# Kernel optimization log

Hardware: AMD Instinct MI355X
Metric: run time of the kernel (lower is better)

## Reference

```python
import jax, jax.numpy as jnp
import numpy as np
from jax import lax

N_HARM = 64
N_BINS = 64
SR = 16000
B, T = 16, 64000


def setup_inputs() -> dict:
    key = jax.random.key(0)
    ks = jax.random.split(key, 12)
    audio = jax.random.normal(ks[0], (B, T), dtype=jnp.float32)
    # realistic fundamental frequencies in [80, 400) Hz
    f0 = 80.0 + 320.0 * jax.random.uniform(ks[1], (B, T), dtype=jnp.float32)
    white_noise = jax.random.normal(ks[2], (B, T), dtype=jnp.float32)
    def wconv(k, o, i, ksz):
        return jax.random.normal(k, (o, i, ksz), dtype=jnp.float32) * (1.0 / np.sqrt(i * ksz))
    w1 = wconv(ks[3], 32, 1, 9); b1 = jnp.zeros((32,), jnp.float32)
    w2 = wconv(ks[4], 64, 32, 9); b2 = jnp.zeros((64,), jnp.float32)
    w3 = wconv(ks[5], 128, 64, 9); b3 = jnp.zeros((128,), jnp.float32)
    wl = jax.random.normal(ks[6], (N_HARM + N_BINS, 128), dtype=jnp.float32) * (1.0 / np.sqrt(128))
    bl = jnp.zeros((N_HARM + N_BINS,), jnp.float32)
    return {"audio": audio, "f0": f0, "white_noise": white_noise,
            "w1": w1, "b1": b1, "w2": w2, "b2": b2, "w3": w3, "b3": b3,
            "wl": wl, "bl": bl}


def _conv1d(x, w, b):
    # x: [B, C_in, T], w: [C_out, C_in, K]; stride 2, pad 4
    y = lax.conv_general_dilated(x, w, window_strides=(2,), padding=[(4, 4)],
                                 dimension_numbers=("NCH", "OIH", "NCH"))
    return jax.nn.relu(y + b[None, :, None])


def reference(audio, f0, white_noise, w1, b1, w2, b2, w3, b3, wl, bl):
    batch, time = audio.shape
    # --- encoder ---
    x = audio[:, None, :]                    # [B, 1, T]
    x = _conv1d(x, w1, b1)                   # [B, 32, T/2]
    x = _conv1d(x, w2, b2)                   # [B, 64, T/4]
    x = _conv1d(x, w3, b3)                   # [B, 128, T/8]
    pooled = x.mean(axis=2)                  # AdaptiveAvgPool1d(1) + Flatten -> [B, 128]
    feats = pooled @ wl.T + bl               # [B, 128]
    # --- harmonic synth ---
    amps = jax.nn.relu(feats[:, :N_HARM])    # [B, H]; constant over time in original
    amps = amps / (amps.sum(axis=1, keepdims=True) + 1e-6)
    t = jnp.linspace(0.0, time / SR, time)   # endpoint-inclusive, as torch.linspace
    harm_idx = jnp.arange(1, N_HARM + 1, dtype=jnp.float32)
    # phase: [B, H, T] = 2*pi * (h * f0) * t
    phase = (2.0 * jnp.pi) * f0[:, None, :] * harm_idx[None, :, None] * t[None, None, :]
    harmonic_audio = jnp.einsum("bh,bht->bt", amps, jnp.sin(phase))
    # --- noise synth ---
    noise_mag = feats[:, N_HARM:]            # [B, n_bins]; mean over time of a constant = itself
    bin_size = time // N_BINS
    shaped = (white_noise.reshape(batch, N_BINS, bin_size) * noise_mag[:, :, None]).reshape(batch, time)
    return harmonic_audio + shaped
```

## Files before the change

### kernel.cpp

```cpp
#include <hip/hip_runtime.h>
#include <hip/hip_bf16.h>
#include <math.h>

typedef unsigned short u16;
typedef _Float16 f16x8 __attribute__((ext_vector_type(8)));
typedef float    f32x16 __attribute__((ext_vector_type(16)));
typedef u16      u16x8  __attribute__((ext_vector_type(8)));
typedef u16      u16x4  __attribute__((ext_vector_type(4)));

#define BATCH 16
#define T0 64000
#define T1 32000
#define T2 16000
#define T3 8000
#define NT3 250
#define NBLKX 32
#define NROWS1 1040

static __device__ __forceinline__ u16 f2h(float f) {
    _Float16 h = (_Float16)f;
    u16 u;
    __builtin_memcpy(&u, &h, 2);
    return u;
}

__global__ __launch_bounds__(256) void prep_w_k(const float* __restrict__ w2,
                                                const float* __restrict__ w3,
                                                u16* __restrict__ a2t,
                                                u16* __restrict__ a3t,
                                                float* __restrict__ pooled) {
    int idx = blockIdx.x * 256 + threadIdx.x;
    if (idx < 18432) {
        int j = idx & 7, o = (idx >> 3) & 63, g = (idx >> 9) & 3, kk = idx >> 11;
        a2t[idx] = f2h(w2[(o * 32 + g * 8 + j) * 9 + kk]);
    } else if (idx < 18432 + 73728) {
        int jdx = idx - 18432;
        int j = jdx & 7, o = (jdx >> 3) & 127, g = (jdx >> 10) & 7, kk = jdx >> 13;
        a3t[jdx] = f2h(w3[(o * 64 + g * 8 + j) * 9 + kk]);
    } else if (idx < 18432 + 73728 + 2048) {
        pooled[idx - 18432 - 73728] = 0.f;
    }
}

__global__ __launch_bounds__(512, 2) void mega_k(const float* __restrict__ audio,
                                                 const float* __restrict__ w1,
                                                 const float* __restrict__ b1,
                                                 const u16* __restrict__ a2t,
                                                 const float* __restrict__ b2,
                                                 const u16* __restrict__ a3t,
                                                 const float* __restrict__ b3,
                                                 float* __restrict__ pooled) {
    __shared__ u16 sm[520 * 64];
    const int tid = threadIdx.x;
    const int b = blockIdx.y;
    const int r0 = blockIdx.x * NT3;
    const int lane = tid & 63, wv = tid >> 6;
    const int ls = lane >> 5, ln = lane & 31;

    {
        const float* ar = audio + (size_t)b * T0;
        #pragma unroll
        for (int rep = 0; rep < 3; ++rep) {
            int l1 = rep * 512 + tid;
            if (l1 >= NROWS1) break;
            int t1 = 4 * r0 - 12 + l1;
            int rr = l1 >> 1, pp = l1 & 1;
            if (t1 < 0 || t1 >= T1) {
                u16x8 z;
                #pragma unroll
                for (int q = 0; q < 8; ++q) z[q] = 0;
                #pragma unroll
                for (int g = 0; g < 4; ++g) {
                    int slot = (pp * 4 + g) ^ (rr & 7);
                    *(u16x8*)(sm + rr * 64 + slot * 8) = z;
                }
            } else {
                int base = 2 * t1 - 4;
                float x[9];
                #pragma unroll
                for (int k = 0; k < 9; ++k) {
                    int t0v = base + k;
                    x[k] = (t0v >= 0 && t0v < T0) ? ar[t0v] : 0.f;
                }
                #pragma unroll
                for (int g = 0; g < 4; ++g) {
                    u16x8 v;
                    #pragma unroll
                    for (int j = 0; j < 8; ++j) {
                        int ch = g * 8 + j;
                        float acc = b1[ch];
                        #pragma unroll
                        for (int k = 0; k < 9; ++k) acc = fmaf(x[k], w1[ch * 9 + k], acc);
                        v[j] = f2h(fmaxf(acc, 0.f));
                    }
                    int slot = (pp * 4 + g) ^ (rr & 7);
                    *(u16x8*)(sm + rr * 64 + slot * 8) = v;
                }
            }
        }
    }
    __syncthreads();

    for (int cc = 0; cc < 2; ++cc) {
        int nl = cc * 256 + 32 * wv + ln;
        f32x16 acc2[2];
        #pragma unroll
        for (int mi = 0; mi < 2; ++mi)
            #pragma unroll
            for (int q = 0; q < 16; ++q) acc2[mi][q] = 0.f;
        f16x8 bfB[2];
        #pragma unroll 3
        for (int kk = 0; kk < 9; ++kk) {
            {
                int rr = nl + (kk >> 1);
                int pp = kk & 1;
                #pragma unroll
                for (int step = 0; step < 2; ++step) {
                    int slot = (pp * 4 + 2 * step + ls) ^ (rr & 7);
                    bfB[step] = *(const f16x8*)(sm + rr * 64 + slot * 8);
                }
            }
            const u16* ap = a2t + kk * 2048;
            #pragma unroll
            for (int step = 0; step < 2; ++step) {
                f16x8 af0 = *(const f16x8*)(ap + (2 * step + ls) * 512 + ln * 8);
                f16x8 af1 = *(const f16x8*)(ap + (2 * step + ls) * 512 + (32 + ln) * 8);
                acc2[0] = __builtin_amdgcn_mfma_f32_32x32x16_f16(af0, bfB[step], acc2[0], 0, 0, 0);
                acc2[1] = __builtin_amdgcn_mfma_f32_32x32x16_f16(af1, bfB[step], acc2[1], 0, 0, 0);
            }
        }
        __syncthreads();
        int l2 = nl;
        int t2 = 2 * r0 - 4 + l2;
        bool valid = (t2 >= 0) && (t2 < T2);
        #pragma unroll
        for (int mi = 0; mi < 2; ++mi)
            #pragma unroll
            for (int q = 0; q < 4; ++q) {
                u16x4 v;
                #pragma unroll
                for (int d = 0; d < 4; ++d) {
                    int o = 32 * mi + 8 * q + 4 * ls + d;
                    float xv = valid ? fmaxf(acc2[mi][4 * q + d] + b2[o], 0.f) : 0.f;
                    v[d] = f2h(xv);
                }
                int gy = 4 * mi + q;
                int sy = gy ^ ((l2 >> 1) & 7);
                *(u16x4*)(sm + l2 * 64 + sy * 8 + ls * 4) = v;
            }
        __syncthreads();
    }

    const int mh = wv & 1, nh = wv >> 1;
    f32x16 acc3[2][2];
    #pragma unroll
    for (int mi = 0; mi < 2; ++mi)
        #pragma unroll
        for (int ni = 0; ni < 2; ++ni)
            #pragma unroll
            for (int q = 0; q < 16; ++q) acc3[mi][ni][q] = 0.f;

    f16x8 bf[2][4];
    #pragma unroll 3
    for (int kk = 0; kk < 9; ++kk) {
        const u16* ap = a3t + kk * 8192;
        {
            #pragma unroll
            for (int ni = 0; ni < 2; ++ni) {
                int nl = 64 * nh + 32 * ni + ln;
                int l2 = 2 * nl + kk;
                int rrC = nl + (kk >> 1);
                #pragma unroll
                for (int step = 0; step < 4; ++step) {
                    int sy = (2 * step + ls) ^ (rrC & 7);
                    bf[ni][step] = *(const f16x8*)(sm + l2 * 64 + sy * 8);
                }
            }
        }
        #pragma unroll
        for (int step = 0; step < 4; ++step) {
            f16x8 af0 = *(const f16x8*)(ap + (2 * step + ls) * 1024 + (64 * mh + ln) * 8);
            f16x8 af1 = *(const f16x8*)(ap + (2 * step + ls) * 1024 + (64 * mh + 32 + ln) * 8);
            #pragma unroll
            for (int ni = 0; ni < 2; ++ni) {
                acc3[0][ni] = __builtin_amdgcn_mfma_f32_32x32x16_f16(af0, bf[ni][step], acc3[0][ni], 0, 0, 0);
                acc3[1][ni] = __builtin_amdgcn_mfma_f32_32x32x16_f16(af1, bf[ni][step], acc3[1][ni], 0, 0, 0);
            }
        }
    }

    float loc[32];
    #pragma unroll
    for (int mi = 0; mi < 2; ++mi)
        #pragma unroll
        for (int r = 0; r < 16; ++r) {
            int o = 64 * mh + 32 * mi + (r & 3) + 8 * (r >> 2) + 4 * ls;
            float bias = b3[o];
            float s = 0.f;
            #pragma unroll
            for (int ni = 0; ni < 2; ++ni) {
                int nl = 64 * nh + 32 * ni + ln;
                float v = fmaxf(acc3[mi][ni][r] + bias, 0.f);
                s += (nl < NT3) ? v : 0.f;
            }
            loc[mi * 16 + r] = s;
        }
    __syncthreads();
    float* smf = (float*)sm;
    #pragma unroll
    for (int mi = 0; mi < 2; ++mi)
        #pragma unroll
        for (int r = 0; r < 16; ++r) {
            int o = 64 * mh + 32 * mi + (r & 3) + 8 * (r >> 2) + 4 * ls;
            smf[nh * 4096 + o * 32 + ln] = loc[mi * 16 + r];
        }
    __syncthreads();
    if (tid < 128) {
        int o = tid;
        float s = 0.f;
        #pragma unroll
        for (int j = 0; j < 32; ++j) {
            int col = (j + o) & 31;
            s += smf[o * 32 + col] + smf[4096 + o * 32 + col]
               + smf[8192 + o * 32 + col] + smf[12288 + o * 32 + col];
        }
        atomicAdd(&pooled[b * 128 + o], s);
    }
}

__global__ __launch_bounds__(128) void feats_k(const float* __restrict__ pooled,
                                               const float* __restrict__ wl,
                                               const float* __restrict__ bl,
                                               float* __restrict__ featbuf) {
    const int b = blockIdx.x;
    const int tid = threadIdx.x;
    __shared__ float pl[128];
    pl[tid] = pooled[b * 128 + tid] * (1.0f / 8000.0f);
    __syncthreads();
    float feat = bl[tid];
    #pragma unroll 8
    for (int i = 0; i < 128; ++i) feat = fmaf(pl[i], wl[tid * 128 + i], feat);
    if (tid < 64) {
        float r = fmaxf(feat, 0.f);
        float s = r;
        #pragma unroll
        for (int off = 32; off > 0; off >>= 1) s += __shfl_xor(s, off);
        featbuf[b * 128 + tid] = r / (s + 1e-6f);
    } else {
        featbuf[b * 128 + tid] = feat;
    }
}

__global__ __launch_bounds__(256) void synth_k(const float* __restrict__ f0,
                                               const float* __restrict__ wn,
                                               const float* __restrict__ featbuf,
                                               float* __restrict__ out) {
    const int tid = threadIdx.x;
    const int b = blockIdx.y;
    __shared__ float sa[64];
    __shared__ float nm[64];
    if (tid < 64) sa[tid] = featbuf[b * 128 + tid];
    else if (tid < 128) nm[tid - 64] = featbuf[b * 128 + tid];
    __syncthreads();

    const int t0v = blockIdx.x * 1024 + tid * 4;
    if (t0v >= T0) return;

    const float4 fv = *(const float4*)(f0 + (size_t)b * T0 + t0v);
    const float4 wv = *(const float4*)(wn + (size_t)b * T0 + t0v);

    float sc[4], sp[4], tc[4], ac[4];
    #pragma unroll
    for (int s = 0; s < 4; ++s) {
        double u = (double)((&fv.x)[s]) * ((double)(t0v + s) * (4.0 / 63999.0));
        float uf = (float)(u - floor(u));
        sc[s] = __builtin_amdgcn_sinf(uf);
        tc[s] = 2.0f * __builtin_amdgcn_cosf(uf);
        sp[s] = 0.f;
        ac[s] = 0.f;
    }
    #pragma unroll
    for (int h = 0; h < 64; ++h) {
        float a = sa[h];
        #pragma unroll
        for (int s = 0; s < 4; ++s) {
            ac[s] = fmaf(a, sc[s], ac[s]);
            float sn = fmaf(tc[s], sc[s], -sp[s]);
            sp[s] = sc[s];
            sc[s] = sn;
        }
    }
    float4 o;
    #pragma unroll
    for (int s = 0; s < 4; ++s)
        (&o.x)[s] = ac[s] + (&wv.x)[s] * nm[(t0v + s) / 1000];
    *(float4*)(out + (size_t)b * T0 + t0v) = o;
}

extern "C" void kernel_launch(void* const* d_in, const int* in_sizes, int n_in,
                              void* d_out, int out_size, void* d_ws, size_t ws_size,
                              hipStream_t stream) {
    const float* audio = (const float*)d_in[0];
    const float* f0    = (const float*)d_in[1];
    const float* wn    = (const float*)d_in[2];
    const float* w1    = (const float*)d_in[3];
    const float* b1    = (const float*)d_in[4];
    const float* w2    = (const float*)d_in[5];
    const float* b2    = (const float*)d_in[6];
    const float* w3    = (const float*)d_in[7];
    const float* b3    = (const float*)d_in[8];
    const float* wl    = (const float*)d_in[9];
    const float* bl    = (const float*)d_in[10];
    float* out = (float*)d_out;

    char* ws = (char*)d_ws;
    float* pooled = (float*)(ws);
    u16* a2t = (u16*)(ws + 8192);
    u16* a3t = (u16*)(ws + 8192 + 36864);
    float* featbuf = (float*)(ws + 8192);

    prep_w_k<<<368, 256, 0, stream>>>(w2, w3, a2t, a3t, pooled);
    mega_k<<<dim3(NBLKX, BATCH), 512, 0, stream>>>(audio, w1, b1, a2t, b2, a3t, b3, pooled);
    feats_k<<<16, 128, 0, stream>>>(pooled, wl, bl, featbuf);
    synth_k<<<dim3((T0 + 1023) / 1024, BATCH), 256, 0, stream>>>(f0, wn, featbuf, out);
}
```

Measured before the change: 130.9 us.

## Fuse feats into mega kernel via last-block counter, merge conv2 chunk loops

Removes the separate feats_k launch by having the last block per batch (detected with an atomic counter) compute the linear layer and amplitude normalization inside mega_k. Conv2's two column chunks are now computed in one loop, so A-fragments are loaded once and reused for both chunks, with a single sync pair. Launch bounds are raised to 4 blocks per SM, which caps registers and may cause spills given the doubled conv2 accumulators. Also reorganizes workspace layout so featbuf no longer aliases a2t.

```diff
diff --git a/kernel.cpp b/kernel.cpp
--- a/kernel.cpp
+++ b/kernel.cpp
@@ -28,7 +28,8 @@
                                                 const float* __restrict__ w3,
                                                 u16* __restrict__ a2t,
                                                 u16* __restrict__ a3t,
-                                                float* __restrict__ pooled) {
+                                                float* __restrict__ pooled,
+                                                int* __restrict__ cnt) {
     int idx = blockIdx.x * 256 + threadIdx.x;
     if (idx < 18432) {
         int j = idx & 7, o = (idx >> 3) & 63, g = (idx >> 9) & 3, kk = idx >> 11;
@@ -39,17 +40,23 @@
         a3t[jdx] = f2h(w3[(o * 64 + g * 8 + j) * 9 + kk]);
     } else if (idx < 18432 + 73728 + 2048) {
         pooled[idx - 18432 - 73728] = 0.f;
-    }
-}
-
-__global__ __launch_bounds__(512, 2) void mega_k(const float* __restrict__ audio,
+    } else if (idx < 18432 + 73728 + 2048 + 16) {
+        cnt[idx - 18432 - 73728 - 2048] = 0;
+    }
+}
+
+__global__ __launch_bounds__(512, 4) void mega_k(const float* __restrict__ audio,
                                                  const float* __restrict__ w1,
                                                  const float* __restrict__ b1,
                                                  const u16* __restrict__ a2t,
                                                  const float* __restrict__ b2,
                                                  const u16* __restrict__ a3t,
                                                  const float* __restrict__ b3,
-                                                 float* __restrict__ pooled) {
+                                                 float* __restrict__ pooled,
+                                                 int* __restrict__ cnt,
+                                                 const float* __restrict__ wl,
+                                                 const float* __restrict__ bl,
+                                                 float* __restrict__ featbuf) {
     __shared__ u16 sm[520 * 64];
     const int tid = threadIdx.x;
     const int b = blockIdx.y;
@@ -101,53 +108,59 @@
     }
     __syncthreads();
 
-    for (int cc = 0; cc < 2; ++cc) {
-        int nl = cc * 256 + 32 * wv + ln;
-        f32x16 acc2[2];
-        #pragma unroll
-        for (int mi = 0; mi < 2; ++mi)
-            #pragma unroll
-            for (int q = 0; q < 16; ++q) acc2[mi][q] = 0.f;
-        f16x8 bfB[2];
+    {
+        f32x16 acc2[2][2];
+        #pragma unroll
+        for (int cc = 0; cc < 2; ++cc)
+            #pragma unroll
+            for (int mi = 0; mi < 2; ++mi)
+                #pragma unroll
+                for (int q = 0; q < 16; ++q) acc2[cc][mi][q] = 0.f;
         #pragma unroll 3
         for (int kk = 0; kk < 9; ++kk) {
-            {
-                int rr = nl + (kk >> 1);
-                int pp = kk & 1;
+            const u16* ap = a2t + kk * 2048;
+            f16x8 af[2][2];
+            #pragma unroll
+            for (int step = 0; step < 2; ++step) {
+                af[step][0] = *(const f16x8*)(ap + (2 * step + ls) * 512 + ln * 8);
+                af[step][1] = *(const f16x8*)(ap + (2 * step + ls) * 512 + (32 + ln) * 8);
+            }
+            int pp = kk & 1, kh = kk >> 1;
+            #pragma unroll
+            for (int cc = 0; cc < 2; ++cc) {
+                int nl = cc * 256 + 32 * wv + ln;
+                int rr = nl + kh;
                 #pragma unroll
                 for (int step = 0; step < 2; ++step) {
                     int slot = (pp * 4 + 2 * step + ls) ^ (rr & 7);
-                    bfB[step] = *(const f16x8*)(sm + rr * 64 + slot * 8);
-                }
-            }
-            const u16* ap = a2t + kk * 2048;
-            #pragma unroll
-            for (int step = 0; step < 2; ++step) {
-                f16x8 af0 = *(const f16x8*)(ap + (2 * step + ls) * 512 + ln * 8);
-                f16x8 af1 = *(const f16x8*)(ap + (2 * step + ls) * 512 + (32 + ln) * 8);
-                acc2[0] = __builtin_amdgcn_mfma_f32_32x32x16_f16(af0, bfB[step], acc2[0], 0, 0, 0);
-                acc2[1] = __builtin_amdgcn_mfma_f32_32x32x16_f16(af1, bfB[step], acc2[1], 0, 0, 0);
+                    f16x8 bfB = *(const f16x8*)(sm + rr * 64 + slot * 8);
+                    acc2[cc][0] = __builtin_amdgcn_mfma_f32_32x32x16_f16(af[step][0], bfB, acc2[cc][0], 0, 0, 0);
+                    acc2[cc][1] = __builtin_amdgcn_mfma_f32_32x32x16_f16(af[step][1], bfB, acc2[cc][1], 0, 0, 0);
+                }
             }
         }
         __syncthreads();
-        int l2 = nl;
-        int t2 = 2 * r0 - 4 + l2;
-        bool valid = (t2 >= 0) && (t2 < T2);
-        #pragma unroll
-        for (int mi = 0; mi < 2; ++mi)
-            #pragma unroll
-            for (int q = 0; q < 4; ++q) {
-                u16x4 v;
-                #pragma unroll
-                for (int d = 0; d < 4; ++d) {
-                    int o = 32 * mi + 8 * q + 4 * ls + d;
-                    float xv = valid ? fmaxf(acc2[mi][4 * q + d] + b2[o], 0.f) : 0.f;
-                    v[d] = f2h(xv);
-                }
-                int gy = 4 * mi + q;
-                int sy = gy ^ ((l2 >> 1) & 7);
-                *(u16x4*)(sm + l2 * 64 + sy * 8 + ls * 4) = v;
-            }
+        #pragma unroll
+        for (int cc = 0; cc < 2; ++cc) {
+            int l2 = cc * 256 + 32 * wv + ln;
+            int t2 = 2 * r0 - 4 + l2;
+            bool valid = (t2 >= 0) && (t2 < T2);
+            #pragma unroll
+            for (int mi = 0; mi < 2; ++mi)
+                #pragma unroll
+                for (int q = 0; q < 4; ++q) {
+                    u16x4 v;
+                    #pragma unroll
+                    for (int d = 0; d < 4; ++d) {
+                        int o = 32 * mi + 8 * q + 4 * ls + d;
+                        float xv = valid ? fmaxf(acc2[cc][mi][4 * q + d] + b2[o], 0.f) : 0.f;
+                        v[d] = f2h(xv);
+                    }
+                    int gy = 4 * mi + q;
+                    int sy = gy ^ ((l2 >> 1) & 7);
+                    *(u16x4*)(sm + l2 * 64 + sy * 8 + ls * 4) = v;
+                }
+        }
         __syncthreads();
     }
 
@@ -226,28 +239,34 @@
         }
         atomicAdd(&pooled[b * 128 + o], s);
     }
-}
-
-__global__ __launch_bounds__(128) void feats_k(const float* __restrict__ pooled,
-                                               const float* __restrict__ wl,
-                                               const float* __restrict__ bl,
-                                               float* __restrict__ featbuf) {
-    const int b = blockIdx.x;
-    const int tid = threadIdx.x;
-    __shared__ float pl[128];
-    pl[tid] = pooled[b * 128 + tid] * (1.0f / 8000.0f);
-    __syncthreads();
-    float feat = bl[tid];
-    #pragma unroll 8
-    for (int i = 0; i < 128; ++i) feat = fmaf(pl[i], wl[tid * 128 + i], feat);
-    if (tid < 64) {
-        float r = fmaxf(feat, 0.f);
-        float s = r;
-        #pragma unroll
-        for (int off = 32; off > 0; off >>= 1) s += __shfl_xor(s, off);
-        featbuf[b * 128 + tid] = r / (s + 1e-6f);
-    } else {
-        featbuf[b * 128 + tid] = feat;
+
+    __threadfence();
+    __syncthreads();
+    int* smi = (int*)sm;
+    if (tid == 0) {
+        int done = atomicAdd(&cnt[b], 1);
+        smi[0] = (done == NBLKX - 1) ? 1 : 0;
+    }
+    __syncthreads();
+    if (smi[0]) {
+        float* pl = (float*)sm + 64;
+        if (tid < 128)
+            pl[tid] = atomicAdd(&pooled[b * 128 + tid], 0.f) * (1.0f / 8000.0f);
+        __syncthreads();
+        if (tid < 128) {
+            float feat = bl[tid];
+            #pragma unroll 8
+            for (int i = 0; i < 128; ++i) feat = fmaf(pl[i], wl[tid * 128 + i], feat);
+            if (tid < 64) {
+                float r = fmaxf(feat, 0.f);
+                float s = r;
+                #pragma unroll
+                for (int off = 32; off > 0; off >>= 1) s += __shfl_xor(s, off);
+                featbuf[b * 128 + tid] = r / (s + 1e-6f);
+            } else {
+                featbuf[b * 128 + tid] = feat;
+            }
+        }
     }
 }
 
@@ -314,13 +333,14 @@
     float* out = (float*)d_out;
 
     char* ws = (char*)d_ws;
-    float* pooled = (float*)(ws);
-    u16* a2t = (u16*)(ws + 8192);
-    u16* a3t = (u16*)(ws + 8192 + 36864);
-    float* featbuf = (float*)(ws + 8192);
-
-    prep_w_k<<<368, 256, 0, stream>>>(w2, w3, a2t, a3t, pooled);
-    mega_k<<<dim3(NBLKX, BATCH), 512, 0, stream>>>(audio, w1, b1, a2t, b2, a3t, b3, pooled);
-    feats_k<<<16, 128, 0, stream>>>(pooled, wl, bl, featbuf);
+    float* pooled  = (float*)(ws);
+    int*   cnt     = (int*)(ws + 8192);
+    float* featbuf = (float*)(ws + 8448);
+    u16*   a2t     = (u16*)(ws + 16640);
+    u16*   a3t     = (u16*)(ws + 16640 + 36864);
+
+    prep_w_k<<<369, 256, 0, stream>>>(w2, w3, a2t, a3t, pooled, cnt);
+    mega_k<<<dim3(NBLKX, BATCH), 512, 0, stream>>>(audio, w1, b1, a2t, b2, a3t, b3,
+                                                   pooled, cnt, wl, bl, featbuf);
     synth_k<<<dim3((T0 + 1023) / 1024, BATCH), 256, 0, stream>>>(f0, wn, featbuf, out);
 }
```

Measured after the change: 181.2 us. +38.3%, slower.
